# Kernel optimization log

Hardware: AMD Instinct MI355X
Metric: run time of the kernel (lower is better)

The kernel has to match this reference:

```python
import jax, jax.numpy as jnp
import numpy as np

G = 16  # self.group
K = 3   # unfold/fold kernel size


def setup_inputs() -> dict:
    key = jax.random.key(0)
    feature = jax.random.normal(key, (2, 128, 192, 192), dtype=jnp.float32)
    return {"feature": feature}


def reference(feature):
    B, C, H, W = feature.shape
    Cg = C // G
    Hm, Wm = H - K + 1, W - K + 1
    L = Hm * Wm

    # --- nn.Unfold(kernel_size=3), all groups at once ---
    # patches[b, c, k, y, x] with k = ki*3 + kj (channel-major flat = c*9 + k)
    slices = [feature[:, :, ki:ki + Hm, kj:kj + Wm] for ki in range(K) for kj in range(K)]
    patches = jnp.stack(slices, axis=2)                 # [B, C, 9, Hm, Wm]
    # per-group series flat dim is Cg*9 (order cg*9+k); chunk(9) -> reshape [9, Cg]
    motif = patches.reshape(B, G, Cg * 9, L).reshape(B, G, 9, Cg, L)  # [B,G,9,Cg,L]

    # --- cdist + diag=inf + argmin (squared distances: same argmin as p=2) ---
    gram = jnp.einsum('bgjcl,bgjdl->bgjcd', motif, motif)   # [B,G,9,Cg,Cg]
    sq = jnp.einsum('bgjcl,bgjcl->bgjc', motif, motif)      # [B,G,9,Cg]
    d2 = sq[..., :, None] + sq[..., None, :] - 2.0 * gram
    eye = jnp.eye(Cg, dtype=bool)
    d2 = jnp.where(eye, jnp.inf, d2)
    nn_idx = jnp.argmin(d2, axis=-1)                        # [B,G,9,Cg] int

    # --- torch.unique loop overwrites motif_new: only the LAST (max) unique
    # index and its count survive ---
    u_max = jnp.max(nn_idx, axis=-1)                        # [B,G,9]
    c_max = jnp.sum(nn_idx == u_max[..., None], axis=-1).astype(feature.dtype)  # [B,G,9]

    motif_nn = jnp.take_along_axis(motif, u_max[..., None, None], axis=3)  # [B,G,9,1,L]
    # float '//' in torch is floor division
    term = jnp.floor(motif * motif_nn * c_max[..., None, None] / Cg)
    # l == 0 branch drops the '+ motif' term
    batch_mask = (jnp.arange(B) != 0).astype(feature.dtype).reshape(B, 1, 1, 1, 1)
    out_ser = motif * batch_mask + term                     # [B,G,9,Cg,L]

    # --- nn.Fold: input layout reinterpreted as (channel, kernel) flat = c*9+k ---
    ser2 = out_ser.reshape(B, G, 9 * Cg, L).reshape(B, G, Cg, 9, Hm, Wm)
    out = jnp.zeros((B, G, Cg, H, W), feature.dtype)
    for k in range(K * K):
        ki, kj = k // K, k % K
        out = out.at[:, :, :, ki:ki + Hm, kj:kj + Wm].add(ser2[:, :, :, k])
    return out.reshape(B, C, H, W)
```

## Files before the change

### kernel.cpp

```cpp
#include <hip/hip_runtime.h>
#include <math.h>

#define BB 2
#define CC 128
#define GG 16
#define CG 8
#define HH 192
#define WW 192
#define HM 190
#define WM 190
#define HWSZ (HH * WW)
#define NTRIPLE (BB * GG * 9)
#define SPLIT 8
#define RREG 24

typedef float float4a __attribute__((ext_vector_type(4), aligned(4)));
typedef float float4v __attribute__((ext_vector_type(4)));

__device__ float g_part[NTRIPLE * SPLIT * 36];
__device__ int g_rel[BB * GG * 72];
__device__ float g_scl[BB * GG * 72];

constexpr bool row_used(int J, int ci, int ki) {
  for (int d = 0; d < 8; ++d) {
    const int f = 8 * J + d;
    if ((f / 9 - (8 * J) / 9) == ci && (f % 9) / 3 == ki) return true;
  }
  return false;
}

template <int J>
__device__ __forceinline__ void gram_region(float* s_ch, int rows, int tid,
                                            float acc[36]) {
  constexpr int CA = (8 * J) / 9;
  constexpr int CB = (8 * J + 7) / 9;
  constexpr int NCH = (CB > CA) ? 2 : 1;

  const int ngrp = rows * 47;
  for (int q = tid; q < ngrp; q += 256) {
    const int ly = q / 47;
    const int x0 = (q % 47) * 4;

    float w[NCH][3][8];
#pragma unroll
    for (int ci = 0; ci < NCH; ++ci) {
#pragma unroll
      for (int ki = 0; ki < 3; ++ki) {
        if (row_used(J, ci, ki)) {
          const float* rp = s_ch + (ci * 26 + ly + ki) * 192 + x0;
          const float4v a = *(const float4v*)rp;
          const float4v bq = *(const float4v*)(rp + 4);
          w[ci][ki][0] = a.x; w[ci][ki][1] = a.y;
          w[ci][ki][2] = a.z; w[ci][ki][3] = a.w;
          w[ci][ki][4] = bq.x; w[ci][ki][5] = bq.y;
          w[ci][ki][6] = bq.z; w[ci][ki][7] = bq.w;
        }
      }
    }
#pragma unroll
    for (int d = 0; d < 8; ++d) {
      const int f = 8 * J + d;
      const int ci = f / 9 - CA;
      const int k = f % 9;
      const int ki = k / 3, kj = k % 3;
      float s = 0.0f;
#pragma unroll
      for (int e = 0; e < 4; ++e) s += w[ci][ki][kj + e] * w[ci][ki][kj + e];
      acc[d] += s;
    }
    int p = 8;
#pragma unroll
    for (int c = 0; c < 8; ++c) {
      const int f1 = 8 * J + c;
      const int ci1 = f1 / 9 - CA;
      const int k1 = f1 % 9;
      const int ki1 = k1 / 3, kj1 = k1 % 3;
#pragma unroll
      for (int d = c + 1; d < 8; ++d) {
        const int f2 = 8 * J + d;
        const int ci2 = f2 / 9 - CA;
        const int k2 = f2 % 9;
        const int ki2 = k2 / 3, kj2 = k2 % 3;
        float s = 0.0f;
#pragma unroll
        for (int e = 0; e < 4; ++e)
          s += w[ci1][ki1][kj1 + e] * w[ci2][ki2][kj2 + e];
        acc[p++] += s;
      }
    }
  }

  const int ncl = rows * 2;
  for (int t = tid; t < ncl; t += 256) {
    const int ly = t / 2;
    const int x = 188 + (t & 1);
    float v[8];
#pragma unroll
    for (int d = 0; d < 8; ++d) {
      const int f = 8 * J + d;
      const int ci = f / 9 - CA;
      const int k = f % 9;
      const int ki = k / 3, kj = k % 3;
      v[d] = s_ch[(ci * 26 + ly + ki) * 192 + x + kj];
    }
#pragma unroll
    for (int d = 0; d < 8; ++d) acc[d] += v[d] * v[d];
    int p = 8;
#pragma unroll
    for (int c = 0; c < 8; ++c)
#pragma unroll
      for (int d = c + 1; d < 8; ++d) acc[p++] += v[c] * v[d];
  }
}

__global__ __launch_bounds__(256, 2) void phase1_kernel(
    const float* __restrict__ feat) {
  const int B = blockIdx.x;
  const int xcd = B & 7;
  const int slot = B >> 3;
  const int unit = xcd * 4 + slot / 72;
  const int rem = slot % 72;
  const int j = rem / 8;
  const int region = rem % 8;
  const int b = unit >> 4;
  const int g = unit & 15;

  const int cA = (8 * j) / 9;
  const int cB = (8 * j + 7) / 9;
  const int nch = (cB > cA) ? 2 : 1;
  const float* pA = feat + (size_t)(b * CC + g * CG + cA) * HWSZ;
  const float* pB = feat + (size_t)(b * CC + g * CG + cB) * HWSZ;

  const int y0 = region * RREG;
  const int rows = (y0 + RREG <= HM) ? RREG : HM - y0;
  const int tid = (int)threadIdx.x;

  __shared__ float s_ch[2 * 26 * 192];

  const int rs = rows + 2;
  const int nst = nch * rs * 48;
  for (int t = tid; t < nst; t += 256) {
    const int ch = t / (rs * 48);
    const int r2 = t % (rs * 48);
    const int row = r2 / 48;
    const int quad = r2 % 48;
    const float4v val =
        *(const float4v*)((ch ? pB : pA) + (y0 + row) * WW + quad * 4);
    *(float4v*)(s_ch + (ch * 26 + row) * 192 + quad * 4) = val;
  }
  __syncthreads();

  float acc[36];
#pragma unroll
  for (int i = 0; i < 36; ++i) acc[i] = 0.0f;

  switch (j) {
    case 0: gram_region<0>(s_ch, rows, tid, acc); break;
    case 1: gram_region<1>(s_ch, rows, tid, acc); break;
    case 2: gram_region<2>(s_ch, rows, tid, acc); break;
    case 3: gram_region<3>(s_ch, rows, tid, acc); break;
    case 4: gram_region<4>(s_ch, rows, tid, acc); break;
    case 5: gram_region<5>(s_ch, rows, tid, acc); break;
    case 6: gram_region<6>(s_ch, rows, tid, acc); break;
    case 7: gram_region<7>(s_ch, rows, tid, acc); break;
    default: gram_region<8>(s_ch, rows, tid, acc); break;
  }

  __syncthreads();
  float* red = s_ch;
  const int lane = tid & 63;
  const int wave = tid >> 6;
#pragma unroll
  for (int i = 0; i < 36; ++i) {
    float v = acc[i];
    for (int o = 32; o > 0; o >>= 1) v += __shfl_down(v, o, 64);
    if (lane == 0) red[i * 4 + wave] = v;
  }
  __syncthreads();
  if (tid < 36) {
    const int tri = unit * 9 + j;
    g_part[(tri * SPLIT + region) * 36 + tid] =
        ((red[tid * 4] + red[tid * 4 + 1]) + red[tid * 4 + 2]) +
        red[tid * 4 + 3];
  }
}

__global__ __launch_bounds__(64) void phase1b_kernel() {
  const int tri = blockIdx.x;
  const int tid = (int)threadIdx.x;
  const int b = tri / (GG * 9);
  const int rem = tri % (GG * 9);
  const int g = rem / 9;
  const int j = rem % 9;

  __shared__ float s_tot[36];
  if (tid < 36) {
    float t = 0.0f;
    for (int s = 0; s < SPLIT; ++s)
      t += g_part[(tri * SPLIT + s) * 36 + tid];
    s_tot[tid] = t;
  }
  __syncthreads();
  if (tid != 0) return;

  float sq[8], gm[8][8];
#pragma unroll
  for (int i = 0; i < 8; ++i) sq[i] = s_tot[i];
  {
    int p = 8;
    for (int c = 0; c < 8; ++c)
      for (int d = c + 1; d < 8; ++d) {
        gm[c][d] = s_tot[p];
        gm[d][c] = s_tot[p];
        ++p;
      }
  }
  int nn[8];
  for (int c = 0; c < 8; ++c) {
    float best = INFINITY;
    int bi = 0;
    for (int d = 0; d < 8; ++d) {
      if (d == c) continue;
      const float d2 = sq[c] + sq[d] - 2.0f * gm[c][d];
      if (d2 < best) {
        best = d2;
        bi = d;
      }
    }
    nn[c] = bi;
  }
  int um = 0;
  for (int c = 0; c < 8; ++c) um = um > nn[c] ? um : nn[c];
  int cnt = 0;
  for (int c = 0; c < 8; ++c) cnt += (nn[c] == um) ? 1 : 0;

  const float sc = (float)cnt * 0.125f;
  const int fn = j * 8 + um;
  const int cn = fn / 9;
  const int kn = fn % 9;
  const int kin = kn / 3, kjn = kn % 3;
  for (int d = 0; d < 8; ++d) {
    const int f = j * 8 + d;
    const int cl = f / 9;
    const int k = f % 9;
    const int ki = k / 3, kj = k % 3;
    const int rel = (cn - cl) * HWSZ + (kin - ki) * WW + (kjn - kj);
    const int tix = (b * GG + g) * 72 + f;
    g_rel[tix] = rel;
    g_scl[tix] = sc;
  }
}

__global__ __launch_bounds__(256) void phase2_main_kernel(
    const float* __restrict__ feat, float* __restrict__ out) {
  const int B = blockIdx.x;
  const int xcd = B & 7;
  const int slot = B >> 3;
  const int unit = xcd * 4 + slot / 144;
  const int r = slot % 144;
  const int cl = r / 18;
  const int blk = r % 18;
  const int plane = unit * 8 + cl;

  const int tbase = unit * 72 + cl * 9;
  int rel[9];
  float scl[9];
#pragma unroll
  for (int k = 0; k < 9; ++k) {
    rel[k] = g_rel[tbase + k];
    scl[k] = g_scl[tbase + k];
  }

  const float* pb = feat + (size_t)plane * HWSZ;
  float* ob = out + (size_t)plane * HWSZ;
  const bool b1 = (unit >= GG);
  const int i0 = blk * 2048 + (int)threadIdx.x * 4;

#pragma unroll
  for (int gidx = 0; gidx < 2; ++gidx) {
    const int inner = i0 + gidx * 1024;
    const int h = inner / WW;
    const int w0 = inner % WW;
    if (h >= 2 && h < HM && w0 >= 4 && w0 < 188) {
      const float* p = pb + inner;
      const float4v v = *(const float4v*)p;
      float4v acc = {0.0f, 0.0f, 0.0f, 0.0f};
#pragma unroll
      for (int k = 0; k < 9; ++k) {
        const float4a n = *(const float4a*)(p + rel[k]);
        const float s = scl[k];
        acc.x += floorf(v.x * n.x * s);
        acc.y += floorf(v.y * n.y * s);
        acc.z += floorf(v.z * n.z * s);
        acc.w += floorf(v.w * n.w * s);
      }
      if (b1) {
        acc.x += 9.0f * v.x;
        acc.y += 9.0f * v.y;
        acc.z += 9.0f * v.z;
        acc.w += 9.0f * v.w;
      }
      *(float4v*)(ob + inner) = acc;
    }
  }
}

__global__ __launch_bounds__(256) void phase2_edge_kernel(
    const float* __restrict__ feat, float* __restrict__ out) {
  const int gid = blockIdx.x * 256 + (int)threadIdx.x;
  const int plane = gid / 2272;
  const int ei = gid % 2272;
  int h, w;
  if (ei < 768) {
    const int r = ei / WW;
    h = (r < 2) ? r : r + 188;
    w = ei % WW;
  } else {
    const int e2 = ei - 768;
    h = 2 + (e2 >> 3);
    const int w8 = e2 & 7;
    w = (w8 < 4) ? w8 : w8 + 184;
  }
  const int g = (plane % CC) >> 3;
  const int cl = (plane % CC) & 7;
  const int tbase = ((plane / CC) * GG + g) * 72 + cl * 9;

  int rel[9];
  float scl[9];
#pragma unroll
  for (int k = 0; k < 9; ++k) {
    rel[k] = g_rel[tbase + k];
    scl[k] = g_scl[tbase + k];
  }

  const int idx = plane * HWSZ + h * WW + w;
  const float* p = feat + idx;
  const float v = *p;
  float acc = 0.0f;
  int nv = 0;
#pragma unroll
  for (int k = 0; k < 9; ++k) {
    const int ki = k / 3, kj = k % 3;
    const int y = h - ki, x = w - kj;
    const bool valid = ((unsigned)y < (unsigned)HM) & ((unsigned)x < (unsigned)WM);
    const int o = valid ? rel[k] : 0;
    const float n = p[o];
    const float fl = floorf(v * n * scl[k]);
    acc += valid ? fl : 0.0f;
    nv += valid ? 1 : 0;
  }
  if (plane >= CC) acc += (float)nv * v;
  out[idx] = acc;
}

extern "C" void kernel_launch(void* const* d_in, const int* in_sizes, int n_in,
                              void* d_out, int out_size, void* d_ws,
                              size_t ws_size, hipStream_t stream) {
  const float* feat = (const float*)d_in[0];
  float* out = (float*)d_out;
  (void)d_ws;
  (void)ws_size;
  (void)in_sizes;
  (void)n_in;
  (void)out_size;

  phase1_kernel<<<NTRIPLE * SPLIT, 256, 0, stream>>>(feat);
  phase1b_kernel<<<NTRIPLE, 64, 0, stream>>>();
  phase2_main_kernel<<<BB * CC * 18, 256, 0, stream>>>(feat, out);
  phase2_edge_kernel<<<2272, 256, 0, stream>>>(feat, out);
}
```

Before: 143.8 us.

## Replace LDS-staged Gram tiles with per-thread register sliding windows over rows

Phase 1 no longer stages rows into shared memory. Each thread now owns a 4-column by 10-row strip and reads rows straight from global memory, keeping a rotating 3-row register window so each loaded row is reused for three kernel offsets. Work is split into 4 blocks per triple instead of 8, with edge columns handled as separate tasks. This removes the LDS fill, its barrier and the per-group LDS reads. In exchange it relies on L1/L2 caching for the overlapping column loads, and the unrolled windows may raise register pressure.

```diff
diff --git a/kernel.cpp b/kernel.cpp
--- a/kernel.cpp
+++ b/kernel.cpp
@@ -11,163 +11,178 @@
 #define WM 190
 #define HWSZ (HH * WW)
 #define NTRIPLE (BB * GG * 9)
-#define SPLIT 8
-#define RREG 24
+#define NSUB 4
+#define YCH 19
+#define CROWS 10
+#define NMAIN (47 * YCH)
+#define NCLEAN (2 * YCH)
+#define NTASK (NMAIN + NCLEAN)
 
 typedef float float4a __attribute__((ext_vector_type(4), aligned(4)));
 typedef float float4v __attribute__((ext_vector_type(4)));
 
-__device__ float g_part[NTRIPLE * SPLIT * 36];
+__device__ float g_part[NTRIPLE * NSUB * 36];
 __device__ int g_rel[BB * GG * 72];
 __device__ float g_scl[BB * GG * 72];
 
-constexpr bool row_used(int J, int ci, int ki) {
-  for (int d = 0; d < 8; ++d) {
-    const int f = 8 * J + d;
-    if ((f / 9 - (8 * J) / 9) == ci && (f % 9) / 3 == ki) return true;
-  }
-  return false;
-}
-
-template <int J>
-__device__ __forceinline__ void gram_region(float* s_ch, int rows, int tid,
-                                            float acc[36]) {
+
+template <int J, int S0, int S1, int S2>
+__device__ __forceinline__ void gram_step(const float* __restrict__ pA,
+                                          const float* __restrict__ pB,
+                                          float (*w)[3][8], int ro,
+                                          float acc[36]) {
   constexpr int CA = (8 * J) / 9;
   constexpr int CB = (8 * J + 7) / 9;
   constexpr int NCH = (CB > CA) ? 2 : 1;
-
-  const int ngrp = rows * 47;
-  for (int q = tid; q < ngrp; q += 256) {
-    const int ly = q / 47;
-    const int x0 = (q % 47) * 4;
-
-    float w[NCH][3][8];
-#pragma unroll
-    for (int ci = 0; ci < NCH; ++ci) {
-#pragma unroll
-      for (int ki = 0; ki < 3; ++ki) {
-        if (row_used(J, ci, ki)) {
-          const float* rp = s_ch + (ci * 26 + ly + ki) * 192 + x0;
-          const float4v a = *(const float4v*)rp;
-          const float4v bq = *(const float4v*)(rp + 4);
-          w[ci][ki][0] = a.x; w[ci][ki][1] = a.y;
-          w[ci][ki][2] = a.z; w[ci][ki][3] = a.w;
-          w[ci][ki][4] = bq.x; w[ci][ki][5] = bq.y;
-          w[ci][ki][6] = bq.z; w[ci][ki][7] = bq.w;
-        }
-      }
-    }
-#pragma unroll
-    for (int d = 0; d < 8; ++d) {
-      const int f = 8 * J + d;
-      const int ci = f / 9 - CA;
-      const int k = f % 9;
-      const int ki = k / 3, kj = k % 3;
+  constexpr int S[3] = {S0, S1, S2};
+
+#pragma unroll
+  for (int ci = 0; ci < NCH; ++ci) {
+    const float* pc = ci ? pB : pA;
+    const float4v a = *(const float4v*)(pc + ro);
+    const float4v bq = *(const float4v*)(pc + ro + 4);
+    w[ci][S2][0] = a.x; w[ci][S2][1] = a.y;
+    w[ci][S2][2] = a.z; w[ci][S2][3] = a.w;
+    w[ci][S2][4] = bq.x; w[ci][S2][5] = bq.y;
+    w[ci][S2][6] = bq.z; w[ci][S2][7] = bq.w;
+  }
+
+#pragma unroll
+  for (int d = 0; d < 8; ++d) {
+    const int f = 8 * J + d;
+    const int ci = f / 9 - CA;
+    const int k = f % 9;
+    const int ki = k / 3, kj = k % 3;
+    float s = 0.0f;
+#pragma unroll
+    for (int e = 0; e < 4; ++e)
+      s += w[ci][S[ki]][kj + e] * w[ci][S[ki]][kj + e];
+    acc[d] += s;
+  }
+  int p = 8;
+#pragma unroll
+  for (int c = 0; c < 8; ++c) {
+    const int f1 = 8 * J + c;
+    const int ci1 = f1 / 9 - CA;
+    const int k1 = f1 % 9;
+    const int ki1 = k1 / 3, kj1 = k1 % 3;
+#pragma unroll
+    for (int d = c + 1; d < 8; ++d) {
+      const int f2 = 8 * J + d;
+      const int ci2 = f2 / 9 - CA;
+      const int k2 = f2 % 9;
+      const int ki2 = k2 / 3, kj2 = k2 % 3;
       float s = 0.0f;
 #pragma unroll
-      for (int e = 0; e < 4; ++e) s += w[ci][ki][kj + e] * w[ci][ki][kj + e];
-      acc[d] += s;
-    }
-    int p = 8;
-#pragma unroll
-    for (int c = 0; c < 8; ++c) {
-      const int f1 = 8 * J + c;
-      const int ci1 = f1 / 9 - CA;
-      const int k1 = f1 % 9;
-      const int ki1 = k1 / 3, kj1 = k1 % 3;
-#pragma unroll
-      for (int d = c + 1; d < 8; ++d) {
-        const int f2 = 8 * J + d;
-        const int ci2 = f2 / 9 - CA;
-        const int k2 = f2 % 9;
-        const int ki2 = k2 / 3, kj2 = k2 % 3;
-        float s = 0.0f;
-#pragma unroll
-        for (int e = 0; e < 4; ++e)
-          s += w[ci1][ki1][kj1 + e] * w[ci2][ki2][kj2 + e];
-        acc[p++] += s;
-      }
-    }
-  }
-
-  const int ncl = rows * 2;
-  for (int t = tid; t < ncl; t += 256) {
-    const int ly = t / 2;
-    const int x = 188 + (t & 1);
-    float v[8];
-#pragma unroll
-    for (int d = 0; d < 8; ++d) {
-      const int f = 8 * J + d;
-      const int ci = f / 9 - CA;
-      const int k = f % 9;
-      const int ki = k / 3, kj = k % 3;
-      v[d] = s_ch[(ci * 26 + ly + ki) * 192 + x + kj];
-    }
-#pragma unroll
-    for (int d = 0; d < 8; ++d) acc[d] += v[d] * v[d];
-    int p = 8;
-#pragma unroll
-    for (int c = 0; c < 8; ++c)
-#pragma unroll
-      for (int d = c + 1; d < 8; ++d) acc[p++] += v[c] * v[d];
+      for (int e = 0; e < 4; ++e)
+        s += w[ci1][S[ki1]][kj1 + e] * w[ci2][S[ki2]][kj2 + e];
+      acc[p++] += s;
+    }
+  }
+}
+
+template <int J>
+__device__ __forceinline__ void gram_main(const float* __restrict__ pA,
+                                          const float* __restrict__ pB,
+                                          int x0, int y0, float acc[36]) {
+  constexpr int CA = (8 * J) / 9;
+  constexpr int CB = (8 * J + 7) / 9;
+  constexpr int NCH = (CB > CA) ? 2 : 1;
+  float w[NCH][3][8];
+
+#pragma unroll
+  for (int ci = 0; ci < NCH; ++ci) {
+    const float* pc = ci ? pB : pA;
+#pragma unroll
+    for (int s = 0; s < 2; ++s) {
+      const float4v a = *(const float4v*)(pc + (y0 + s) * WW + x0);
+      const float4v bq = *(const float4v*)(pc + (y0 + s) * WW + x0 + 4);
+      w[ci][s][0] = a.x; w[ci][s][1] = a.y;
+      w[ci][s][2] = a.z; w[ci][s][3] = a.w;
+      w[ci][s][4] = bq.x; w[ci][s][5] = bq.y;
+      w[ci][s][6] = bq.z; w[ci][s][7] = bq.w;
+    }
+  }
+
+  int ro = (y0 + 2) * WW + x0;
+#pragma unroll
+  for (int t = 0; t < 3; ++t) {
+    gram_step<J, 0, 1, 2>(pA, pB, w, ro, acc); ro += WW;
+    gram_step<J, 1, 2, 0>(pA, pB, w, ro, acc); ro += WW;
+    gram_step<J, 2, 0, 1>(pA, pB, w, ro, acc); ro += WW;
+  }
+  gram_step<J, 0, 1, 2>(pA, pB, w, ro, acc);
+}
+
+template <int J>
+__device__ __forceinline__ void task_work(const float* __restrict__ pA,
+                                          const float* __restrict__ pB,
+                                          int m, float acc[36]) {
+  if (m < NMAIN) {
+    const int ychk = m / 47;
+    const int xi = m % 47;
+    gram_main<J>(pA, pB, xi * 4, ychk * CROWS, acc);
+  } else if (m < NTASK) {
+    constexpr int CA = (8 * J) / 9;
+    const int c2 = m - NMAIN;
+    const int x = 188 + (c2 & 1);
+    const int y0 = (c2 >> 1) * CROWS;
+    for (int y = y0; y < y0 + CROWS; ++y) {
+      float v[8];
+#pragma unroll
+      for (int d = 0; d < 8; ++d) {
+        const int f = 8 * J + d;
+        const int ci = f / 9 - CA;
+        const int k = f % 9;
+        const int ki = k / 3, kj = k % 3;
+        v[d] = (ci ? pB : pA)[(y + ki) * WW + x + kj];
+      }
+#pragma unroll
+      for (int d = 0; d < 8; ++d) acc[d] += v[d] * v[d];
+      int p = 8;
+#pragma unroll
+      for (int c = 0; c < 8; ++c)
+#pragma unroll
+        for (int d = c + 1; d < 8; ++d) acc[p++] += v[c] * v[d];
+    }
   }
 }
 
 __global__ __launch_bounds__(256, 2) void phase1_kernel(
     const float* __restrict__ feat) {
   const int B = blockIdx.x;
-  const int xcd = B & 7;
-  const int slot = B >> 3;
-  const int unit = xcd * 4 + slot / 72;
-  const int rem = slot % 72;
-  const int j = rem / 8;
-  const int region = rem % 8;
-  const int b = unit >> 4;
-  const int g = unit & 15;
+  const int tri = B >> 2;
+  const int sub = B & 3;
+  const int b = tri / (GG * 9);
+  const int rem = tri % (GG * 9);
+  const int g = rem / 9;
+  const int j = rem % 9;
 
   const int cA = (8 * j) / 9;
   const int cB = (8 * j + 7) / 9;
-  const int nch = (cB > cA) ? 2 : 1;
   const float* pA = feat + (size_t)(b * CC + g * CG + cA) * HWSZ;
   const float* pB = feat + (size_t)(b * CC + g * CG + cB) * HWSZ;
 
-  const int y0 = region * RREG;
-  const int rows = (y0 + RREG <= HM) ? RREG : HM - y0;
   const int tid = (int)threadIdx.x;
-
-  __shared__ float s_ch[2 * 26 * 192];
-
-  const int rs = rows + 2;
-  const int nst = nch * rs * 48;
-  for (int t = tid; t < nst; t += 256) {
-    const int ch = t / (rs * 48);
-    const int r2 = t % (rs * 48);
-    const int row = r2 / 48;
-    const int quad = r2 % 48;
-    const float4v val =
-        *(const float4v*)((ch ? pB : pA) + (y0 + row) * WW + quad * 4);
-    *(float4v*)(s_ch + (ch * 26 + row) * 192 + quad * 4) = val;
-  }
-  __syncthreads();
+  const int m = sub * 256 + tid;
 
   float acc[36];
 #pragma unroll
   for (int i = 0; i < 36; ++i) acc[i] = 0.0f;
 
   switch (j) {
-    case 0: gram_region<0>(s_ch, rows, tid, acc); break;
-    case 1: gram_region<1>(s_ch, rows, tid, acc); break;
-    case 2: gram_region<2>(s_ch, rows, tid, acc); break;
-    case 3: gram_region<3>(s_ch, rows, tid, acc); break;
-    case 4: gram_region<4>(s_ch, rows, tid, acc); break;
-    case 5: gram_region<5>(s_ch, rows, tid, acc); break;
-    case 6: gram_region<6>(s_ch, rows, tid, acc); break;
-    case 7: gram_region<7>(s_ch, rows, tid, acc); break;
-    default: gram_region<8>(s_ch, rows, tid, acc); break;
-  }
-
-  __syncthreads();
-  float* red = s_ch;
+    case 0: task_work<0>(pA, pB, m, acc); break;
+    case 1: task_work<1>(pA, pB, m, acc); break;
+    case 2: task_work<2>(pA, pB, m, acc); break;
+    case 3: task_work<3>(pA, pB, m, acc); break;
+    case 4: task_work<4>(pA, pB, m, acc); break;
+    case 5: task_work<5>(pA, pB, m, acc); break;
+    case 6: task_work<6>(pA, pB, m, acc); break;
+    case 7: task_work<7>(pA, pB, m, acc); break;
+    default: task_work<8>(pA, pB, m, acc); break;
+  }
+
+  __shared__ float red[36 * 4];
   const int lane = tid & 63;
   const int wave = tid >> 6;
 #pragma unroll
@@ -178,8 +193,7 @@
   }
   __syncthreads();
   if (tid < 36) {
-    const int tri = unit * 9 + j;
-    g_part[(tri * SPLIT + region) * 36 + tid] =
+    g_part[(tri * NSUB + sub) * 36 + tid] =
         ((red[tid * 4] + red[tid * 4 + 1]) + red[tid * 4 + 2]) +
         red[tid * 4 + 3];
   }
@@ -196,8 +210,8 @@
   __shared__ float s_tot[36];
   if (tid < 36) {
     float t = 0.0f;
-    for (int s = 0; s < SPLIT; ++s)
-      t += g_part[(tri * SPLIT + s) * 36 + tid];
+    for (int s = 0; s < NSUB; ++s)
+      t += g_part[(tri * NSUB + s) * 36 + tid];
     s_tot[tid] = t;
   }
   __syncthreads();
@@ -364,7 +378,7 @@
   (void)n_in;
   (void)out_size;
 
-  phase1_kernel<<<NTRIPLE * SPLIT, 256, 0, stream>>>(feat);
+  phase1_kernel<<<NTRIPLE * NSUB, 256, 0, stream>>>(feat);
   phase1b_kernel<<<NTRIPLE, 64, 0, stream>>>();
   phase2_main_kernel<<<BB * CC * 18, 256, 0, stream>>>(feat, out);
   phase2_edge_kernel<<<2272, 256, 0, stream>>>(feat, out);
```

Result: slower. 204.8 us (+42.5%).
